# Kernel optimization log

Measured on AMD Instinct MI355X. Metric: run time of the kernel, lower is better.

The kernel has to match this reference:

```python
import jax, jax.numpy as jnp
import numpy as np

N, E, CS = 8, 256, 8
L2, M2 = 2048, 1024
L1 = M2 * CS            # 8192 tokens at depth-1
M1 = 4096
LLAST = M1 * CS         # 32768 tokens at last layer
S = L2 + L1 + LLAST     # 43008
NUM_VOCAB = 16
RES = 64


def _mixed_values(key, n, L, M):
    # values in {1,3}, with exactly M positions per row set to the 'mixed' token 2
    k1, k2 = jax.random.split(key)
    base = jax.random.randint(k1, (n, L), 0, 2) * 2 + 1
    perms = jax.vmap(lambda k: jax.random.permutation(k, L))(jax.random.split(k2, n))
    mask = jnp.zeros((n, L), bool).at[jnp.arange(n)[:, None], perms[:, :M]].set(True)
    return jnp.where(mask, 2, base).astype(jnp.int32)


def setup_inputs() -> dict:
    key = jax.random.key(0)
    ks = jax.random.split(key, 16)
    v2 = _mixed_values(ks[0], N, L2, M2)
    v1 = _mixed_values(ks[1], N, L1, M1)
    vl = jax.random.randint(ks[2], (N, LLAST), 1, 4).astype(jnp.int32)
    value = jnp.concatenate([v2, v1, vl], axis=1)
    depth = jnp.concatenate([
        jnp.full((N, L2), 4, jnp.int32),
        jnp.full((N, L1), 5, jnp.int32),
        jnp.full((N, LLAST), 6, jnp.int32)], axis=1)
    pos = jax.random.randint(ks[3], (N, S, 3), 0, RES).astype(jnp.int32)
    x = jax.random.normal(ks[4], (N, L2 // CS, E), jnp.float32)
    s = 0.02
    return {
        'x': x, 'value': value, 'depth': depth, 'pos': pos,
        'W2': jax.random.normal(ks[5], (E, E, CS), jnp.float32) * s,
        'b2': jax.random.normal(ks[6], (E,), jnp.float32) * s,
        'W1': jax.random.normal(ks[7], (E, E, CS), jnp.float32) * s,
        'b1': jax.random.normal(ks[8], (E,), jnp.float32) * s,
        'W0': jax.random.normal(ks[9], (E, E, CS), jnp.float32) * s,
        'b0': jax.random.normal(ks[10], (E,), jnp.float32) * s,
        'emb': jax.random.normal(ks[11], (3, RES, E), jnp.float32) * s,
        'lin_w': jax.random.normal(ks[12], (E, NUM_VOCAB + 1), jnp.float32) * s,
        'lin_b': jax.random.normal(ks[13], (NUM_VOCAB + 1,), jnp.float32) * s,
    }


def _deconv(h, W, b):
    # ConvTranspose1d with kernel_size == stride == CS: each input token emits CS outputs
    n, t, e = h.shape
    cs = W.shape[2]
    return jnp.einsum('nti,iok->ntko', h, W).reshape(n, t * cs, e) + b


def _compact(y, mask, M):
    # per-row: rows of y where mask, packed to the front (stable), zero padded to M rows
    T = y.shape[1]
    if mask.shape[1] < T:
        mask = jnp.pad(mask, ((0, 0), (0, T - mask.shape[1])))
    else:
        mask = mask[:, :T]
    order = jnp.argsort(jnp.where(mask, 0, 1), axis=1, stable=True)
    g = jnp.take_along_axis(y, order[:, :M, None], axis=1)
    keep = jnp.arange(M)[None, :] < jnp.sum(mask, axis=1)[:, None]
    return jnp.where(keep[:, :, None], g, 0.0)


def reference(x, value, depth, pos, W2, b2, W1, b1, W0, b0, emb, lin_w, lin_b):
    max_depth = int(jnp.max(depth))
    len_1 = jnp.sum(depth == max_depth - 1, axis=1)
    len_2 = jnp.sum(depth == max_depth - 2, axis=1)
    L1_ = int(jnp.max(len_1)); L2_ = int(jnp.max(len_2))
    j2 = jnp.arange(L2_); j1 = jnp.arange(L1_)
    val_2 = jnp.where(j2[None, :] < len_2[:, None], value[:, :L2_], 0)
    idx1 = jnp.clip(len_2[:, None] + j1[None, :], 0, value.shape[1] - 1)
    val_1 = jnp.where(j1[None, :] < len_1[:, None], jnp.take_along_axis(value, idx1, axis=1), 0)
    mix_1 = jnp.sum(val_1 == 2, axis=1); mix_2 = jnp.sum(val_2 == 2, axis=1)
    M1_ = int(jnp.max(mix_1)); M2_ = int(jnp.max(mix_2))

    y_2 = _deconv(x, W2, b2)                 # [N, T''*cs, E]
    x_1 = _compact(y_2, val_2 == 2, M2_)     # gather mixed depth-2 positions
    y_1 = _deconv(x_1, W1, b1)
    x_0 = _compact(y_1, val_1 == 2, M1_)     # gather mixed depth-1 positions
    y_0 = _deconv(x_0, W0, b0)               # [N, M1_*cs, E]

    len_last = int(jnp.sum(depth[0] == max_depth))  # uniform across batch (torch slicing requires it)
    p = pos[:, -len_last:]                   # [N, len_last, 3]
    enc = emb[0][p[..., 0]] + emb[1][p[..., 1]] + emb[2][p[..., 2]]
    y_0 = y_0 + enc
    return y_0 @ lin_w + lin_b
```

## Files before the change

### kernel.cpp

```cpp
#include <hip/hip_runtime.h>
#include <cstdint>
#include <cstddef>

#define SEQ     43008
#define LASTOFF 10240
#define NV      17

typedef __bf16 bf16x8 __attribute__((ext_vector_type(8)));
typedef float  f32x4  __attribute__((ext_vector_type(4)));

typedef __attribute__((address_space(1))) const void gv_t;
typedef __attribute__((address_space(3))) void       lv_t;

__device__ __forceinline__ ushort f2bf(float f) {
    union { float f; unsigned u; } x; x.f = f;
    unsigned r = x.u + 0x7FFFu + ((x.u >> 16) & 1u);
    return (ushort)(r >> 16);
}
__device__ __forceinline__ float bf2f(ushort h) {
    union { unsigned u; float f; } x; x.u = ((unsigned)h) << 16;
    return x.f;
}

__device__ __forceinline__ void stage_tile_w(char* ldsbase, const ushort* src,
                                             int row0, int k0, int nch, int wv,
                                             int nwv, int lane)
{
    int sub  = lane >> 3;
    int col8 = (lane & 7) ^ sub;
    const ushort* g0 = src + (size_t)(row0 + sub) * 256 + k0 + (col8 << 3);
    for (int ch = wv; ch < nch; ch += nwv) {
        const ushort* g = g0 + ((size_t)(ch << 3)) * 256;
        __builtin_amdgcn_global_load_lds((gv_t*)g, (lv_t*)(ldsbase + (ch << 10)), 16, 0, 0);
    }
}

__device__ __forceinline__ bf16x8 frag64(const char* lds, int row, int kk, int lane) {
    int r = row + (lane & 15);
    int byte = (r << 7) + ((kk + ((lane >> 4) << 3)) << 1);
    byte ^= (r & 7) << 4;
    return *(const bf16x8*)(lds + byte);
}

__global__ __launch_bounds__(256) void prep_main(
    const float* __restrict__ x, const float* __restrict__ W2,
    const float* __restrict__ W1, const float* __restrict__ W0,
    const float* __restrict__ lin_w, const int* __restrict__ value,
    const float* __restrict__ emb, const float* __restrict__ b0,
    const float* __restrict__ lin_b,
    ushort* __restrict__ xb, ushort* __restrict__ Wb2T,
    ushort* __restrict__ W1n, ushort* __restrict__ W0n,
    int* __restrict__ dest2,
    int* __restrict__ packT, int* __restrict__ cnt1,
    float* __restrict__ embLp)
{
    __shared__ __align__(16) char sm[33792];
    const int b = blockIdx.x;
    const int tid = threadIdx.x;

    if (b < 192) {
        int s   = b >> 6;
        int rem = b & 63;
        int i0  = (rem >> 3) << 5;
        int o0  = (rem & 7) << 5;
        const float* W = (s == 0) ? W2 : ((s == 1) ? W1 : W0);
        float* tl = (float*)sm;
        #pragma unroll
        for (int q = 0; q < 8; ++q) {
            int fid = (q << 8) + tid;
            int ri  = fid >> 6;
            int f   = (fid & 63) << 2;
            float4 v = *(const float4*)(W + (size_t)(i0 + ri) * 2048 + o0 * 8 + f);
            int ol = f >> 3;
            int c0 = f & 7;
            tl[((c0 + 0) * 32 + ol) * 33 + ri] = v.x;
            tl[((c0 + 1) * 32 + ol) * 33 + ri] = v.y;
            tl[((c0 + 2) * 32 + ol) * 33 + ri] = v.z;
            tl[((c0 + 3) * 32 + ol) * 33 + ri] = v.w;
        }
        __syncthreads();
        int seg = tid & 3;
        if (s >= 1) {
            ushort* Wn = (s == 1) ? W1n : W0n;
            #pragma unroll
            for (int it = 0; it < 4; ++it) {
                int rk = (it << 6) + (tid >> 2);
                int c = rk >> 5, ii = rk & 31;
                ushort v8[8];
                #pragma unroll
                for (int u = 0; u < 8; ++u)
                    v8[u] = f2bf(tl[(c * 32 + (seg << 3) + u) * 33 + ii]);
                *(int4*)(Wn + (c << 16) + (i0 + ii) * 256 + o0 + (seg << 3)) =
                    *(const int4*)v8;
            }
        } else {
            #pragma unroll
            for (int it = 0; it < 4; ++it) {
                int rk = (it << 6) + (tid >> 2);
                int j  = ((rk >> 5) << 8) + o0 + (rk & 31);
                ushort v8[8];
                #pragma unroll
                for (int u = 0; u < 8; ++u)
                    v8[u] = f2bf(tl[rk * 33 + (seg << 3) + u]);
                *(int4*)(Wb2T + ((size_t)j << 8) + i0 + (seg << 3)) =
                    *(const int4*)v8;
            }
        }
    } else if (b < 448) {
        int i8 = (((b - 192) << 8) + tid) << 3;
        float4 a  = *(const float4*)(x + i8);
        float4 bb = *(const float4*)(x + i8 + 4);
        ushort v[8] = { f2bf(a.x), f2bf(a.y), f2bf(a.z), f2bf(a.w),
                        f2bf(bb.x), f2bf(bb.y), f2bf(bb.z), f2bf(bb.w) };
        *(int4*)(xb + i8) = *(const int4*)v;
    } else if (b < 456) {
        int n    = b - 448;
        int base = n * SEQ;
        int* dst = dest2 + n * 2048;
        int cnt = 0;
        int vloc[8];
        #pragma unroll
        for (int i = 0; i < 8; ++i) {
            vloc[i] = value[base + tid * 8 + i];
            cnt += (vloc[i] == 2);
        }
        int* s = (int*)sm;
        s[tid] = cnt;
        __syncthreads();
        for (int off = 1; off < 256; off <<= 1) {
            int v = (tid >= off) ? s[tid - off] : 0;
            __syncthreads();
            s[tid] += v;
            __syncthreads();
        }
        int run = s[tid] - cnt;
        #pragma unroll
        for (int i = 0; i < 8; ++i) {
            int d = -1;
            if (vloc[i] == 2 && run < 1024) { d = run; ++run; }
            dst[tid * 8 + i] = d;
        }
    } else if (b < 464) {
        int n    = b - 456;
        int base = n * SEQ + 2048;
        int (*s8)[8] = (int(*)[8])sm;
        int cnt8[8] = {0,0,0,0,0,0,0,0};
        int vloc[32];
        #pragma unroll
        for (int i = 0; i < 32; ++i) {
            vloc[i] = value[base + tid * 32 + i];
            cnt8[i & 7] += (vloc[i] == 2);
        }
        #pragma unroll
        for (int k = 0; k < 8; ++k) s8[tid][k] = cnt8[k];
        __syncthreads();
        for (int off = 1; off < 256; off <<= 1) {
            int v[8];
            #pragma unroll
            for (int k = 0; k < 8; ++k) v[k] = (tid >= off) ? s8[tid - off][k] : 0;
            __syncthreads();
            #pragma unroll
            for (int k = 0; k < 8; ++k) s8[tid][k] += v[k];
            __syncthreads();
        }
        int runK[8], runTot = 0;
        #pragma unroll
        for (int k = 0; k < 8; ++k) { runK[k] = s8[tid][k] - cnt8[k]; runTot += runK[k]; }
        #pragma unroll
        for (int i = 0; i < 32; ++i) {
            if (vloc[i] == 2) {
                int k  = i & 7;
                int tp = (tid * 32 + i) >> 3;
                packT[(((n << 3) + k) << 10) + runK[k]] = (runTot << 16) | tp;
                runK[k]++; runTot++;
            }
        }
        if (tid < 8) cnt1[(n << 3) + tid] = s8[255][tid];
    } else {
        int idx = b - 464;
        int jd  = idx >> 6;
        int p   = idx & 63;
        float* er = (float*)sm;
        float* ps = er + 256;
        float e = emb[jd * 16384 + p * 256 + tid];
        if (jd == 0) e += b0[tid];
        er[tid] = e;
        __syncthreads();
        if (tid < 136) {
            int v = tid >> 3, part = tid & 7;
            const float* lw = lin_w + v;
            float s = 0.f;
            int o0 = part << 5;
            #pragma unroll 8
            for (int o = o0; o < o0 + 32; ++o)
                s = fmaf(er[o], lw[o * NV], s);
            ps[tid] = s;
        }
        __syncthreads();
        if (tid < 20) {
            float acc = 0.f;
            if (tid < NV) {
                #pragma unroll
                for (int q = 0; q < 8; ++q) acc += ps[tid * 8 + q];
                if (jd == 0) acc += lin_b[tid];
            }
            embLp[jd * 1280 + p * 20 + tid] = acc;
        }
    }
}

__global__ __launch_bounds__(256) void g2h(
    const ushort* __restrict__ A, const ushort* __restrict__ BT,
    const float* __restrict__ bias, const int* __restrict__ dest,
    ushort* __restrict__ Xout,
    const ushort* __restrict__ W0n, const float* __restrict__ lin_w,
    const ushort* __restrict__ W1n, const float* __restrict__ b1,
    ushort* __restrict__ Hf, float* __restrict__ K1f)
{
    extern __shared__ __align__(16) char smem[];
    const int tid = threadIdx.x;
    const int lane = tid & 63, wv = tid >> 6;

    if (blockIdx.x >= 64) {
        const int bx = blockIdx.x - 64;
        const int r0 = (bx & 15) << 7;
        const int c0 = (bx >> 4) << 7;
        const int wm = (wv >> 1) << 6;
        const int wn = (wv & 1) << 6;

        f32x4 acc[4][4] = {};

        stage_tile_w(smem,         A,  r0, 0, 16, wv, 4, lane);
        stage_tile_w(smem + 16384, BT, c0, 0, 16, wv, 4, lane);
        __syncthreads();

        for (int kt = 0; kt < 4; ++kt) {
            char* cb = smem + ((kt & 1) << 15);
            if (kt < 3) {
                char* nb = smem + (((kt + 1) & 1) << 15);
                int k0n = (kt + 1) << 6;
                stage_tile_w(nb,         A,  r0, k0n, 16, wv, 4, lane);
                stage_tile_w(nb + 16384, BT, c0, k0n, 16, wv, 4, lane);
            }
            #pragma unroll
            for (int ks = 0; ks < 2; ++ks) {
                int kk = ks << 5;
                bf16x8 af[4], bfr[4];
                #pragma unroll
                for (int i = 0; i < 4; ++i) af[i]  = frag64(cb, wm + i * 16, kk, lane);
                #pragma unroll
                for (int i = 0; i < 4; ++i) bfr[i] = frag64(cb + 16384, wn + i * 16, kk, lane);
                #pragma unroll
                for (int mi = 0; mi < 4; ++mi)
                    #pragma unroll
                    for (int ni = 0; ni < 4; ++ni)
                        acc[mi][ni] = __builtin_amdgcn_mfma_f32_16x16x32_bf16(
                            af[mi], bfr[ni], acc[mi][ni], 0, 0, 0);
            }
            __syncthreads();
        }

        const int obase = c0 & 255;
        const int cdx   = c0 >> 8;
        float bv[4];
        #pragma unroll
        for (int ni = 0; ni < 4; ++ni)
            bv[ni] = bias[obase + wn + ni * 16 + (lane & 15)];

        ushort* Cs = (ushort*)smem;
        #pragma unroll
        for (int mi = 0; mi < 4; ++mi)
            #pragma unroll
            for (int ni = 0; ni < 4; ++ni)
                #pragma unroll
                for (int r = 0; r < 4; ++r) {
                    int row = wm + mi * 16 + ((lane >> 4) << 2) + r;
                    int col = wn + ni * 16 + (lane & 15);
                    Cs[row * 136 + col] = f2bf(acc[mi][ni][r] + bv[ni]);
                }
        __syncthreads();

        for (int p = 0; p < 8; ++p) {
            int row = p * 16 + (tid >> 4);
            int gr  = r0 + row;
            int n   = gr >> 8, t = gr & 255;
            int d   = dest[n * 2048 + t * 8 + cdx];
            if (d >= 0) {
                int4 v = *(const int4*)&Cs[row * 136 + ((tid & 15) << 3)];
                *(int4*)&Xout[(((size_t)n * 1024 + d) << 8) + obase + ((tid & 15) << 3)] = v;
            }
        }
        return;
    }

    const int idx = blockIdx.x;
    const int cp  = idx >> 3, cf = idx & 7;

    ushort* Gs  = (ushort*)smem;
    char*   Bs  = smem + 16384;
    char*   lwA = smem + 49152;

    for (int j = tid; j < 4096; j += 256) ((int*)lwA)[j] = 0;
    __syncthreads();
    {
        int kt = tid >> 6, kq = tid & 63;
        const float* lsrc = lin_w + tid * NV;
        #pragma unroll
        for (int v = 0; v < NV; ++v) {
            int byte = (v << 7) + (kq << 1);
            byte ^= (v & 7) << 4;
            *(ushort*)(lwA + (kt << 12) + byte) = f2bf(lsrc[v]);
        }
    }
    __syncthreads();

    const ushort* W0c = W0n + ((size_t)cf << 16);
    f32x4 acc[2][16];
    {
        f32x4 z = {0.f, 0.f, 0.f, 0.f};
        #pragma unroll
        for (int mi = 0; mi < 2; ++mi)
            #pragma unroll
            for (int ni = 0; ni < 16; ++ni) acc[mi][ni] = z;
    }
    for (int kt = 0; kt < 4; ++kt) {
        stage_tile_w(Bs, W0c, 0, kt << 6, 32, wv, 4, lane);
        __syncthreads();
        #pragma unroll
        for (int ks = 0; ks < 2; ++ks) {
            int kk = ks << 5;
            bf16x8 a0 = frag64(lwA + (kt << 12), 0,  kk, lane);
            bf16x8 a1 = frag64(lwA + (kt << 12), 16, kk, lane);
            #pragma unroll
            for (int ni = 0; ni < 16; ++ni) {
                bf16x8 bfr = frag64(Bs, ni << 4, kk, lane);
                acc[0][ni] = __builtin_amdgcn_mfma_f32_16x16x32_bf16(a0, bfr, acc[0][ni], 0, 0, 0);
                acc[1][ni] = __builtin_amdgcn_mfma_f32_16x16x32_bf16(a1, bfr, acc[1][ni], 0, 0, 0);
            }
        }
        __syncthreads();
    }

    #pragma unroll
    for (int mi = 0; mi < 2; ++mi)
        #pragma unroll
        for (int ni = 0; ni < 16; ++ni)
            #pragma unroll
            for (int r = 0; r < 4; ++r) {
                int v = (mi << 4) + ((lane >> 4) << 2) + r;
                int o = (ni << 4) + (lane & 15);
                int byte = (v << 7) + ((o & 63) << 1);
                byte ^= (v & 7) << 4;
                *(ushort*)((char*)Gs + ((o >> 6) << 12) + byte) = f2bf(acc[mi][ni][r]);
            }
    __syncthreads();

    if (cp == 0) {
        float bo = b1[tid];
        int kt = tid >> 6, kq = tid & 63;
        float p[NV];
        #pragma unroll
        for (int v = 0; v < NV; ++v) {
            int byte = (v << 7) + (kq << 1);
            byte ^= (v & 7) << 4;
            p[v] = bo * bf2f(*(const ushort*)((const char*)Gs + (kt << 12) + byte));
        }
        #pragma unroll
        for (int off = 32; off >= 1; off >>= 1)
            #pragma unroll
            for (int v = 0; v < NV; ++v)
                p[v] += __shfl_xor(p[v], off);
        float* Ks = (float*)lwA;
        if (lane == 0)
            #pragma unroll
            for (int v = 0; v < NV; ++v) Ks[wv * NV + v] = p[v];
        __syncthreads();
        if (tid < NV)
            K1f[cf * NV + tid] = Ks[tid] + Ks[NV + tid] + Ks[2 * NV + tid] + Ks[3 * NV + tid];
        if (cf == 7 && tid >= 136 && tid < 144) K1f[tid] = 0.f;
        __syncthreads();
    }

    const ushort* Wb1 = W1n + ((size_t)cp << 16);
    {
        f32x4 z = {0.f, 0.f, 0.f, 0.f};
        #pragma unroll
        for (int mi = 0; mi < 2; ++mi)
            #pragma unroll
            for (int ni = 0; ni < 16; ++ni) acc[mi][ni] = z;
    }
    for (int kt = 0; kt < 4; ++kt) {
        stage_tile_w(Bs, Wb1, 0, kt << 6, 32, wv, 4, lane);
        __syncthreads();
        #pragma unroll
        for (int ks = 0; ks < 2; ++ks) {
            int kk = ks << 5;
            bf16x8 a0 = frag64((char*)Gs + (kt << 12), 0,  kk, lane);
            bf16x8 a1 = frag64((char*)Gs + (kt << 12), 16, kk, lane);
            #pragma unroll
            for (int ni = 0; ni < 16; ++ni) {
                bf16x8 bfr = frag64(Bs, ni << 4, kk, lane);
                acc[0][ni] = __builtin_amdgcn_mfma_f32_16x16x32_bf16(a0, bfr, acc[0][ni], 0, 0, 0);
                acc[1][ni] = __builtin_amdgcn_mfma_f32_16x16x32_bf16(a1, bfr, acc[1][ni], 0, 0, 0);
            }
        }
        __syncthreads();
    }

    #pragma unroll
    for (int mi = 0; mi < 2; ++mi)
        #pragma unroll
        for (int ni = 0; ni < 16; ++ni)
            #pragma unroll
            for (int r = 0; r < 4; ++r) {
                int v = (mi << 4) + ((lane >> 4) << 2) + r;
                if (v < NV) {
                    int i = (ni << 4) + (lane & 15);
                    Hf[cp * 36864 + (cf * NV + v) * 256 + i] = f2bf(acc[mi][ni][r]);
                }
            }
    if (cf == 7)
        for (int j = tid; j < 2048; j += 256)
            Hf[cp * 36864 + 136 * 256 + j] = 0;
}

__global__ __launch_bounds__(256) void fused_out(
    const ushort* __restrict__ X1, const ushort* __restrict__ Hf,
    const float* __restrict__ embLp, const float* __restrict__ K1f,
    const int* __restrict__ packT, const int* __restrict__ cnt1,
    const int* __restrict__ pos, float* __restrict__ out)
{
    extern __shared__ __align__(16) char smem[];

    const int tid  = threadIdx.x;
    const int lane = tid & 63, wv = tid >> 6;
    const int bb = blockIdx.x;
    const int n  = bb >> 3, cp = bb & 7;
    const int t0 = blockIdx.y << 6;
    const int cnt = cnt1[bb];
    if (t0 >= cnt) return;
    const int cntL = min(64, cnt - t0);

    const int sub  = lane >> 3;
    const int col8 = (lane & 7) ^ sub;
    const int* pbase = packT + (bb << 10);
    int Ta = pbase[t0 + (wv << 3) + sub] & 1023;
    int Tb = pbase[t0 + ((wv + 4) << 3) + sub] & 1023;
    const ushort* ga0 = X1 + ((size_t)((n << 10) + Ta) << 8) + (col8 << 3);
    const ushort* gb0 = X1 + ((size_t)((n << 10) + Tb) << 8) + (col8 << 3);

    float* embLs = (float*)(smem + 53248);
    for (int i = tid; i < 3840; i += 256) embLs[i] = embLp[i];
    float* K1s = (float*)(smem + 68608);
    if (tid < 144) K1s[tid] = K1f[tid];
    int* Ds = (int*)(smem + 69184);
    if (tid < 64) Ds[tid] = (pbase[t0 + tid] >> 16) & 4095;

    const ushort* Hb = Hf + cp * 36864;

    __builtin_amdgcn_global_load_lds((gv_t*)ga0, (lv_t*)(smem + (wv << 10)), 16, 0, 0);
    __builtin_amdgcn_global_load_lds((gv_t*)gb0, (lv_t*)(smem + ((wv + 4) << 10)), 16, 0, 0);
    stage_tile_w(smem + 8192, Hb, 0, 0, 18, wv, 4, lane);
    __syncthreads();

    f32x4 acc[9] = {};
    for (int kt = 0; kt < 4; ++kt) {
        char* cb = smem + (kt & 1) * 26624;
        if (kt < 3) {
            char* nb = smem + ((kt + 1) & 1) * 26624;
            int k0n = (kt + 1) << 6;
            __builtin_amdgcn_global_load_lds((gv_t*)(ga0 + k0n), (lv_t*)(nb + (wv << 10)), 16, 0, 0);
            __builtin_amdgcn_global_load_lds((gv_t*)(gb0 + k0n), (lv_t*)(nb + ((wv + 4) << 10)), 16, 0, 0);
            stage_tile_w(nb + 8192, Hb, 0, k0n, 18, wv, 4, lane);
        }
        #pragma unroll
        for (int ks = 0; ks < 2; ++ks) {
            int kk = ks << 5;
            bf16x8 af = frag64(cb, wv << 4, kk, lane);
            #pragma unroll
            for (int ni = 0; ni < 9; ++ni) {
                bf16x8 bfr = frag64(cb + 8192, ni << 4, kk, lane);
                acc[ni] = __builtin_amdgcn_mfma_f32_16x16x32_bf16(af, bfr, acc[ni], 0, 0, 0);
            }
        }
        __syncthreads();
    }

    float* Cs = (float*)smem;
    #pragma unroll
    for (int ni = 0; ni < 9; ++ni) {
        int col = (ni << 4) + (lane & 15);
        if (col < 136) {
            #pragma unroll
            for (int r = 0; r < 4; ++r) {
                int row = (wv << 4) + ((lane >> 4) << 2) + r;
                Cs[row * 136 + col] = acc[ni][r];
            }
        }
    }
    __syncthreads();

    #pragma unroll
    for (int rr = 0; rr < 2; ++rr) {
        int rl = tid * 2 + rr;
        int r  = rl >> 3, c = rl & 7;
        int prow = n * SEQ + LASTOFF + (Ds[r] << 3) + c;
        const int* pp = pos + 3 * prow;
        const float* e0 = embLs +        pp[0] * 20;
        const float* e1 = embLs + 1280 + pp[1] * 20;
        const float* e2 = embLs + 2560 + pp[2] * 20;
        const float* k1 = K1s + c * 17;
        float* cr = Cs + rl * 17;
        #pragma unroll
        for (int v4 = 0; v4 < 16; v4 += 4) {
            float4 a = *(const float4*)(e0 + v4);
            float4 bq = *(const float4*)(e1 + v4);
            float4 cq = *(const float4*)(e2 + v4);
            cr[v4 + 0] += a.x + bq.x + cq.x + k1[v4 + 0];
            cr[v4 + 1] += a.y + bq.y + cq.y + k1[v4 + 1];
            cr[v4 + 2] += a.z + bq.z + cq.z + k1[v4 + 2];
            cr[v4 + 3] += a.w + bq.w + cq.w + k1[v4 + 3];
        }
        cr[16] += e0[16] + e1[16] + e2[16] + k1[16];
    }
    __syncthreads();

    for (int i4 = tid; i4 < 2176; i4 += 256) {
        int r  = (i4 * 1928) >> 16;
        int fo = i4 - r * 34;
        if (r < cntL) {
            *(float4*)(out + ((size_t)((n << 12) + Ds[r])) * 136 + (fo << 2)) =
                *(const float4*)(Cs + r * 136 + (fo << 2));
        }
    }
}

extern "C" void kernel_launch(void* const* d_in, const int* in_sizes, int n_in,
                              void* d_out, int out_size, void* d_ws, size_t ws_size,
                              hipStream_t stream)
{
    (void)in_sizes; (void)n_in; (void)out_size; (void)ws_size;
    const float* x     = (const float*)d_in[0];
    const int*   value = (const int*)d_in[1];
    const int*   pos   = (const int*)d_in[3];
    const float* W2    = (const float*)d_in[4];
    const float* b2    = (const float*)d_in[5];
    const float* W1    = (const float*)d_in[6];
    const float* b1    = (const float*)d_in[7];
    const float* W0    = (const float*)d_in[8];
    const float* b0    = (const float*)d_in[9];
    const float* emb   = (const float*)d_in[10];
    const float* lin_w = (const float*)d_in[11];
    const float* lin_b = (const float*)d_in[12];
    float* out = (float*)d_out;

    char* ws = (char*)d_ws;
    ushort* Wb2T  = (ushort*)(ws);
    ushort* W0n   = (ushort*)(ws + 2097152);
    ushort* W1n   = (ushort*)(ws + 3145728);
    ushort* xb    = (ushort*)(ws + 4194304);
    int*    dest2 = (int*)   (ws + 5242880);
    int*    cnt1  = (int*)   (ws + 5308416);
    int*    packT = (int*)   (ws + 5308672);
    ushort* x1b   = (ushort*)(ws + 5570816);
    float*  embLp = (float*) (ws + 9838848);
    ushort* Hf    = (ushort*)(ws + 9854208);
    float*  K1f   = (float*) (ws + 10444032);

    prep_main<<<656, 256, 0, stream>>>(x, W2, W1, W0, lin_w, value,
                                       emb, b0, lin_b,
                                       xb, Wb2T, W1n, W0n, dest2, packT, cnt1, embLp);
    g2h<<<320, 256, 65536, stream>>>(xb, Wb2T, b2, dest2, x1b,
                                     W0n, lin_w, W1n, b1, Hf, K1f);
    fused_out<<<dim3(64, 12), 256, 69632, stream>>>(x1b, Hf, embLp, K1f,
                                                    packT, cnt1, pos, out);
}
```

Measured before the change: 56.16 us.

## Register-prefetch weight tiles in g2h and move depth-1 scan blocks into g2h

The W0/W1 tile staging in the g2h head blocks now goes through registers. The next k-tile's global loads are issued before the current tile's MFMAs, and the loaded data is written to LDS afterwards, replacing the synchronous global_load_lds followed by a barrier. The first tile's load is also overlapped with the lin_w setup and with the previous GEMM's epilogue. Separately, the 8 per-batch prefix-scan blocks that build packT/cnt1 move from prep_main into 8 extra g2h blocks, shortening the prep kernel's tail. The cost is higher register pressure from the 8 int4 prefetch registers alongside the 32 accumulators, plus an extra barrier per k-step.

```diff
diff --git a/kernel.cpp b/kernel.cpp
--- a/kernel.cpp
+++ b/kernel.cpp
@@ -35,6 +35,25 @@
     }
 }
 
+__device__ __forceinline__ void stage_regs_load(int4* regs, const ushort* src,
+                                                int row0, int k0, int nch,
+                                                int wv, int nwv, int lane)
+{
+    int sub  = lane >> 3;
+    int col8 = (lane & 7) ^ sub;
+    const ushort* g0 = src + (size_t)(row0 + sub) * 256 + k0 + (col8 << 3);
+    int r = 0;
+    for (int ch = wv; ch < nch; ch += nwv, ++r)
+        regs[r] = *(const int4*)(g0 + ((size_t)(ch << 3)) * 256);
+}
+__device__ __forceinline__ void stage_regs_write(char* ldsbase, const int4* regs,
+                                                 int nch, int wv, int nwv, int lane)
+{
+    int r = 0;
+    for (int ch = wv; ch < nch; ch += nwv, ++r)
+        *(int4*)(ldsbase + (ch << 10) + lane * 16) = regs[r];
+}
+
 __device__ __forceinline__ bf16x8 frag64(const char* lds, int row, int kk, int lane) {
     int r = row + (lane & 15);
     int byte = (r << 7) + ((kk + ((lane >> 4) << 3)) << 1);
@@ -50,9 +69,7 @@
     const float* __restrict__ lin_b,
     ushort* __restrict__ xb, ushort* __restrict__ Wb2T,
     ushort* __restrict__ W1n, ushort* __restrict__ W0n,
-    int* __restrict__ dest2,
-    int* __restrict__ packT, int* __restrict__ cnt1,
-    float* __restrict__ embLp)
+    int* __restrict__ dest2, float* __restrict__ embLp)
 {
     __shared__ __align__(16) char sm[33792];
     const int b = blockIdx.x;
@@ -140,44 +157,8 @@
             if (vloc[i] == 2 && run < 1024) { d = run; ++run; }
             dst[tid * 8 + i] = d;
         }
-    } else if (b < 464) {
-        int n    = b - 456;
-        int base = n * SEQ + 2048;
-        int (*s8)[8] = (int(*)[8])sm;
-        int cnt8[8] = {0,0,0,0,0,0,0,0};
-        int vloc[32];
-        #pragma unroll
-        for (int i = 0; i < 32; ++i) {
-            vloc[i] = value[base + tid * 32 + i];
-            cnt8[i & 7] += (vloc[i] == 2);
-        }
-        #pragma unroll
-        for (int k = 0; k < 8; ++k) s8[tid][k] = cnt8[k];
-        __syncthreads();
-        for (int off = 1; off < 256; off <<= 1) {
-            int v[8];
-            #pragma unroll
-            for (int k = 0; k < 8; ++k) v[k] = (tid >= off) ? s8[tid - off][k] : 0;
-            __syncthreads();
-            #pragma unroll
-            for (int k = 0; k < 8; ++k) s8[tid][k] += v[k];
-            __syncthreads();
-        }
-        int runK[8], runTot = 0;
-        #pragma unroll
-        for (int k = 0; k < 8; ++k) { runK[k] = s8[tid][k] - cnt8[k]; runTot += runK[k]; }
-        #pragma unroll
-        for (int i = 0; i < 32; ++i) {
-            if (vloc[i] == 2) {
-                int k  = i & 7;
-                int tp = (tid * 32 + i) >> 3;
-                packT[(((n << 3) + k) << 10) + runK[k]] = (runTot << 16) | tp;
-                runK[k]++; runTot++;
-            }
-        }
-        if (tid < 8) cnt1[(n << 3) + tid] = s8[255][tid];
     } else {
-        int idx = b - 464;
+        int idx = b - 456;
         int jd  = idx >> 6;
         int p   = idx & 63;
         float* er = (float*)sm;
@@ -215,11 +196,52 @@
     ushort* __restrict__ Xout,
     const ushort* __restrict__ W0n, const float* __restrict__ lin_w,
     const ushort* __restrict__ W1n, const float* __restrict__ b1,
-    ushort* __restrict__ Hf, float* __restrict__ K1f)
+    ushort* __restrict__ Hf, float* __restrict__ K1f,
+    const int* __restrict__ value, int* __restrict__ packT,
+    int* __restrict__ cnt1)
 {
     extern __shared__ __align__(16) char smem[];
     const int tid = threadIdx.x;
     const int lane = tid & 63, wv = tid >> 6;
+
+    if (blockIdx.x >= 320) {
+        int n    = blockIdx.x - 320;
+        int base = n * SEQ + 2048;
+        int (*s8)[8] = (int(*)[8])smem;
+        int cnt8[8] = {0,0,0,0,0,0,0,0};
+        int vloc[32];
+        #pragma unroll
+        for (int i = 0; i < 32; ++i) {
+            vloc[i] = value[base + tid * 32 + i];
+            cnt8[i & 7] += (vloc[i] == 2);
+        }
+        #pragma unroll
+        for (int k = 0; k < 8; ++k) s8[tid][k] = cnt8[k];
+        __syncthreads();
+        for (int off = 1; off < 256; off <<= 1) {
+            int v[8];
+            #pragma unroll
+            for (int k = 0; k < 8; ++k) v[k] = (tid >= off) ? s8[tid - off][k] : 0;
+            __syncthreads();
+            #pragma unroll
+            for (int k = 0; k < 8; ++k) s8[tid][k] += v[k];
+            __syncthreads();
+        }
+        int runK[8], runTot = 0;
+        #pragma unroll
+        for (int k = 0; k < 8; ++k) { runK[k] = s8[tid][k] - cnt8[k]; runTot += runK[k]; }
+        #pragma unroll
+        for (int i = 0; i < 32; ++i) {
+            if (vloc[i] == 2) {
+                int k  = i & 7;
+                int tp = (tid * 32 + i) >> 3;
+                packT[(((n << 3) + k) << 10) + runK[k]] = (runTot << 16) | tp;
+                runK[k]++; runTot++;
+            }
+        }
+        if (tid < 8) cnt1[(n << 3) + tid] = s8[255][tid];
+        return;
+    }
 
     if (blockIdx.x >= 64) {
         const int bx = blockIdx.x - 64;
@@ -300,6 +322,10 @@
     char*   Bs  = smem + 16384;
     char*   lwA = smem + 49152;
 
+    int4 regs[8];
+    const ushort* W0c = W0n + ((size_t)cf << 16);
+    stage_regs_load(regs, W0c, 0, 0, 32, wv, 4, lane);
+
     for (int j = tid; j < 4096; j += 256) ((int*)lwA)[j] = 0;
     __syncthreads();
     {
@@ -312,9 +338,9 @@
             *(ushort*)(lwA + (kt << 12) + byte) = f2bf(lsrc[v]);
         }
     }
+    stage_regs_write(Bs, regs, 32, wv, 4, lane);
     __syncthreads();
 
-    const ushort* W0c = W0n + ((size_t)cf << 16);
     f32x4 acc[2][16];
     {
         f32x4 z = {0.f, 0.f, 0.f, 0.f};
@@ -324,8 +350,8 @@
             for (int ni = 0; ni < 16; ++ni) acc[mi][ni] = z;
     }
     for (int kt = 0; kt < 4; ++kt) {
-        stage_tile_w(Bs, W0c, 0, kt << 6, 32, wv, 4, lane);
-        __syncthreads();
+        if (kt < 3)
+            stage_regs_load(regs, W0c, 0, (kt + 1) << 6, 32, wv, 4, lane);
         #pragma unroll
         for (int ks = 0; ks < 2; ++ks) {
             int kk = ks << 5;
@@ -339,8 +365,14 @@
             }
         }
         __syncthreads();
-    }
-
+        if (kt < 3) {
+            stage_regs_write(Bs, regs, 32, wv, 4, lane);
+            __syncthreads();
+        }
+    }
+
+    const ushort* Wb1 = W1n + ((size_t)cp << 16);
+    stage_regs_load(regs, Wb1, 0, 0, 32, wv, 4, lane);
     #pragma unroll
     for (int mi = 0; mi < 2; ++mi)
         #pragma unroll
@@ -381,7 +413,9 @@
         __syncthreads();
     }
 
-    const ushort* Wb1 = W1n + ((size_t)cp << 16);
+    stage_regs_write(Bs, regs, 32, wv, 4, lane);
+    __syncthreads();
+
     {
         f32x4 z = {0.f, 0.f, 0.f, 0.f};
         #pragma unroll
@@ -390,8 +424,8 @@
             for (int ni = 0; ni < 16; ++ni) acc[mi][ni] = z;
     }
     for (int kt = 0; kt < 4; ++kt) {
-        stage_tile_w(Bs, Wb1, 0, kt << 6, 32, wv, 4, lane);
-        __syncthreads();
+        if (kt < 3)
+            stage_regs_load(regs, Wb1, 0, (kt + 1) << 6, 32, wv, 4, lane);
         #pragma unroll
         for (int ks = 0; ks < 2; ++ks) {
             int kk = ks << 5;
@@ -405,6 +439,10 @@
             }
         }
         __syncthreads();
+        if (kt < 3) {
+            stage_regs_write(Bs, regs, 32, wv, 4, lane);
+            __syncthreads();
+        }
     }
 
     #pragma unroll
@@ -567,11 +605,12 @@
     ushort* Hf    = (ushort*)(ws + 9854208);
     float*  K1f   = (float*) (ws + 10444032);
 
-    prep_main<<<656, 256, 0, stream>>>(x, W2, W1, W0, lin_w, value,
+    prep_main<<<648, 256, 0, stream>>>(x, W2, W1, W0, lin_w, value,
                                        emb, b0, lin_b,
-                                       xb, Wb2T, W1n, W0n, dest2, packT, cnt1, embLp);
-    g2h<<<320, 256, 65536, stream>>>(xb, Wb2T, b2, dest2, x1b,
-                                     W0n, lin_w, W1n, b1, Hf, K1f);
+                                       xb, Wb2T, W1n, W0n, dest2, embLp);
+    g2h<<<328, 256, 65536, stream>>>(xb, Wb2T, b2, dest2, x1b,
+                                     W0n, lin_w, W1n, b1, Hf, K1f,
+                                     value, packT, cnt1);
     fused_out<<<dim3(64, 12), 256, 69632, stream>>>(x1b, Hf, embLp, K1f,
                                                     packT, cnt1, pos, out);
 }
```

Result: slower. 80.99 us (+44.2%).
